# Performance work log

Hardware: AMD Instinct MI355X
Metric: run time of the kernel (lower is better)

## Reference

```python
import jax, jax.numpy as jnp
import numpy as np
from jax import lax

BN_EPS = 1e-5


def conv_bn_relu(x, W, g, b, m, v):
    # 3x3 conv, pad=1, stride=1, no bias; then inference-mode BN; then ReLU
    y = lax.conv_general_dilated(x, W, (1, 1), 'SAME',
                                 dimension_numbers=('NCHW', 'OIHW', 'NCHW'))
    scale = g / jnp.sqrt(v + BN_EPS)
    y = y * scale[None, :, None, None] + (b - m * scale)[None, :, None, None]
    return jax.nn.relu(y)


def shifted_windows(y, d, pad_val):
    # y: [n,c,h,w] -> [k*k, n, c, h, w] of all spatial shifts within radius d
    n, c, h, w = y.shape
    yp = jnp.pad(y, ((0, 0), (0, 0), (d, d), (d, d)), constant_values=pad_val)
    k = 2 * d + 1
    return jnp.stack([yp[:, :, i:i + h, j:j + w] for i in range(k) for j in range(k)], axis=0)


def setup_inputs() -> dict:
    key = jax.random.key(0)
    ks = jax.random.split(key, 16)
    n_clip, n, C_in, H, W = 2, 2, 512, 64, 64
    emb_dim, fc_dim, num_class = 256, 128, 124

    def bn_params(k, c):
        k1, k2, k3, k4 = jax.random.split(k, 4)
        return (jax.random.uniform(k1, (c,)) + 0.5,
                jax.random.normal(k2, (c,)) * 0.1,
                jax.random.normal(k3, (c,)) * 0.1,
                jax.random.uniform(k4, (c,)) + 0.5)

    emb_g, emb_b, emb_m, emb_v = bn_params(ks[0], emb_dim)
    emb2_g, emb2_b, emb2_m, emb2_v = bn_params(ks[1], fc_dim)
    return {
        'clip_embs': jax.random.normal(ks[2], (n_clip * n, C_in, H, W), dtype=jnp.float32),
        'clip_num': 2,
        'emb_W': jax.random.normal(ks[3], (emb_dim, C_in, 3, 3), dtype=jnp.float32) * 0.02,
        'emb_g': emb_g, 'emb_b': emb_b, 'emb_m': emb_m, 'emb_v': emb_v,
        'emb2_W': jax.random.normal(ks[4], (fc_dim, C_in, 3, 3), dtype=jnp.float32) * 0.02,
        'emb2_g': emb2_g, 'emb2_b': emb2_b, 'emb2_m': emb2_m, 'emb2_v': emb2_v,
        'last_W': jax.random.normal(ks[5], (num_class, emb_dim, 1, 1), dtype=jnp.float32) * 0.05,
        'last_b': jnp.zeros((num_class,), dtype=jnp.float32),
    }


MAX_DISTANCES = (2,)
TEMP = 1.0


def reference(clip_embs, clip_num, emb_W, emb_g, emb_b, emb_m, emb_v,
              emb2_W, emb2_g, emb2_b, emb2_m, emb2_v, last_W, last_b):
    # emb_2 features used for the local cost volume (fc_dim channels)
    clip_emb2 = conv_bn_relu(clip_embs, emb2_W, emb2_g, emb2_b, emb2_m, emb2_v)
    chunks2 = jnp.split(clip_emb2, clip_num, axis=0)
    c2 = chunks2[-1]                      # current frame, [n, fc_dim, h, w]
    others2 = chunks2[:-1]

    x2 = jnp.sum(c2 * c2, axis=1)         # [n,h,w]

    all_weights = []                       # per other clip: per max_distance softmax weights
    for other in others2:
        y2 = jnp.sum(other * other, axis=1, keepdims=True)  # [n,1,h,w]
        w_list = []
        for d in MAX_DISTANCES:
            k = 2 * d + 1
            y_sh = shifted_windows(other, d, 0.0)            # [k2,n,c,h,w]
            y2_sh = shifted_windows(y2, d, 1e20)[:, :, 0]    # [k2,n,h,w]
            cross = jnp.einsum('nchw,onchw->onhw', c2, y_sh)
            dist = x2[None] + y2_sh - 2.0 * cross            # [k2,n,h,w] squared L2
            # distsoftmax branch: softmax over the k*k window of 1/(dist*temp+1e-5)
            w_ = jax.nn.softmax(1.0 / (dist * TEMP + 1e-5), axis=0)
            w_list.append(w_)
        all_weights.append(w_list)

    # emb features (emb_dim channels) that get warped
    clip_emb_s = conv_bn_relu(clip_embs, emb_W, emb_g, emb_b, emb_m, emb_v)
    chunks_s = jnp.split(clip_emb_s, clip_num, axis=0)
    c_img = chunks_s[-1]                   # [n, emb_dim, h, w]
    others_s = chunks_s[:-1]

    final_emb = [c_img]
    for other, w_list in zip(others_s, all_weights):
        warp_fs = []
        for d, w_ in zip(MAX_DISTANCES, w_list):
            k = 2 * d + 1
            o_sh = shifted_windows(other, d, 0.0)            # [k2,n,c,h,w]
            # weighted sum over window, then avgpool over k*k -> divide by k*k
            warp = jnp.einsum('onchw,onhw->nchw', o_sh, w_) / (k * k)
            warp_fs.append(warp)
        final_emb.append(jnp.mean(jnp.stack(warp_fs, axis=-1), axis=-1))

    # linear_combine=False: mean over the clip embeddings
    final_fea = jnp.mean(jnp.stack(final_emb, axis=-1), axis=-1)

    # last_layer: dropout (eval -> identity) + 1x1 conv
    logits = jnp.einsum('nchw,oc->nohw', final_fea, last_W[:, :, 0, 0]) + last_b[None, :, None, None]
    x = jax.nn.log_softmax(logits, axis=1)
    return (x, clip_emb2)
```

## Files before the change

### kernel.cpp

```cpp
#include <hip/hip_runtime.h>
#include <hip/hip_bf16.h>
#include <stdint.h>


typedef float v4f __attribute__((ext_vector_type(4)));
typedef __bf16 v8bf __attribute__((ext_vector_type(8)));
typedef unsigned short u16;
typedef unsigned int u32;
typedef u16 u16x8 __attribute__((ext_vector_type(8)));

constexpr size_t XH_OFF  = 0;
constexpr size_t XH_BYTES = (size_t)4*66*66*512*2;
constexpr size_t WT_OFF  = XH_OFF + XH_BYTES;
constexpr size_t WT_BYTES = (size_t)9*16*24*64*8*2;
constexpr size_t FS_OFF  = WT_OFF + WT_BYTES;
constexpr size_t FS_BYTES = (size_t)4*68*68*256*2;
constexpr size_t F2_OFF  = FS_OFF + FS_BYTES;
constexpr size_t F2_BYTES = (size_t)4*68*68*128*4;
constexpr size_t Y2_OFF  = F2_OFF + F2_BYTES;
constexpr size_t Y2_BYTES = (size_t)2*68*68*4;
constexpr size_t FEA_OFF = Y2_OFF + Y2_BYTES;
constexpr size_t FEA_BYTES = (size_t)2*4096*256*2;
constexpr size_t WL_OFF  = FEA_OFF + FEA_BYTES;
constexpr size_t WL_BYTES = (size_t)128*256*2;
constexpr size_t SC_OFF  = WL_OFF + WL_BYTES;
constexpr size_t WS_TOTAL = SC_OFF + 768*4;

__device__ __forceinline__ float bf2f(u16 h) { return __uint_as_float(((u32)h) << 16); }
__device__ __forceinline__ u16 f2bf(float f) {
  u32 u = __float_as_uint(f);
  return (u16)((u + 0x7fffu + ((u >> 16) & 1u)) >> 16);
}

__device__ __forceinline__ void gld16(const void* g, const void* l) {
  __builtin_amdgcn_global_load_lds(
      (const __attribute__((address_space(1))) void*)(uintptr_t)g,
      (__attribute__((address_space(3))) void*)(u32)(uintptr_t)l,
      16, 0, 0);
}

__global__ void k_init(const float* __restrict__ eg, const float* __restrict__ eb,
                       const float* __restrict__ em, const float* __restrict__ ev,
                       const float* __restrict__ e2g, const float* __restrict__ e2b,
                       const float* __restrict__ e2m, const float* __restrict__ e2v,
                       const float* __restrict__ lw,
                       u16* __restrict__ Xh, u16* __restrict__ Fs, float* __restrict__ F2,
                       float* __restrict__ Y2, u16* __restrict__ Wl,
                       float* __restrict__ sc, float* __restrict__ bi) {
  const u32 N0 = 4u * 260u * 64u;
  const u32 N1 = 4u * 528u * 32u;
  const u32 N2 = 4u * 528u * 32u;
  const u32 N3 = 2u * 68u * 68u;
  const u32 N4 = 4096u;
  const u32 N5 = 384u;
  const u32 TOT = N0 + N1 + N2 + N3 + N4 + N5;
  const u16x8 z8 = {0,0,0,0,0,0,0,0};
  for (u32 i = blockIdx.x * 256u + threadIdx.x; i < TOT; i += gridDim.x * 256u) {
    if (i < N0) {
      const u32 img = i / (260u * 64u);
      const u32 rem = i - img * (260u * 64u);
      const u32 r = rem >> 6, ch8 = rem & 63u;
      u32 prow, pcol;
      if (r < 132u) { prow = (r >= 66u) ? 65u : 0u; pcol = r - ((r >= 66u) ? 66u : 0u); }
      else { const u32 rr = r - 132u; prow = 1u + (rr >> 1); pcol = (rr & 1u) * 65u; }
      *(u16x8*)(Xh + ((size_t)((img * 66u + prow) * 66u + pcol)) * 512u + ch8 * 8u) = z8;
    } else if (i < N0 + N1 + N2) {
      const bool isF2 = (i >= N0 + N1);
      const u32 j = isF2 ? (i - N0 - N1) : (i - N0);
      const u32 img = j / (528u * 32u);
      const u32 rem = j - img * (528u * 32u);
      const u32 r = rem >> 5, cg = rem & 31u;
      u32 prow, pcol;
      if (r < 272u) { const u32 q = r / 68u; prow = (q < 2u) ? q : q + 64u; pcol = r - q * 68u; }
      else { const u32 rr = r - 272u; prow = 2u + (rr >> 2); const u32 c = rr & 3u; pcol = (c < 2u) ? c : c + 64u; }
      if (isF2) {
        const float4 zf = {0.f, 0.f, 0.f, 0.f};
        *(float4*)(F2 + ((size_t)((img * 68u + prow) * 68u + pcol)) * 128u + cg * 4u) = zf;
      } else {
        *(u16x8*)(Fs + ((size_t)((img * 68u + prow) * 68u + pcol)) * 256u + cg * 8u) = z8;
      }
    } else if (i < N0 + N1 + N2 + N3) {
      const u32 j = i - N0 - N1 - N2;
      const u32 n = j / 4624u, rc = j - n * 4624u;
      const u32 rr = rc / 68u, cc = rc - rr * 68u;
      const bool interior = (rr >= 2u && rr < 66u && cc >= 2u && cc < 66u);
      Y2[j] = interior ? 0.f : 1e20f;
    } else if (i < N0 + N1 + N2 + N3 + N4) {
      const u32 j = i - N0 - N1 - N2 - N3;
      const u32 row = j >> 5, c8 = (j & 31u) * 8u;
      u16x8 o;
      #pragma unroll
      for (int k = 0; k < 8; ++k) o[k] = (row < 124u) ? f2bf(lw[row * 256u + c8 + k]) : (u16)0;
      *(u16x8*)(Wl + (size_t)row * 256u + c8) = o;
    } else {
      const u32 id = i - N0 - N1 - N2 - N3 - N4;
      float g, b, m, v;
      if (id < 256u) { g = eg[id]; b = eb[id]; m = em[id]; v = ev[id]; }
      else { const u32 q = id - 256u; g = e2g[q]; b = e2b[q]; m = e2m[q]; v = e2v[q]; }
      const float s = g / sqrtf(v + 1e-5f);
      sc[id] = s;
      bi[id] = b - m * s;
    }
  }
}

__global__ __launch_bounds__(256) void k_prep_x(const float* __restrict__ X, u16* __restrict__ Xh) {
  __shared__ __align__(16) float tile[64 * 65];
  const int tid = threadIdx.x;
  const int n = blockIdx.x >> 7;
  const int rem = blockIdx.x & 127;
  const int h = rem >> 1, chalf = rem & 1;
  const int wq = tid >> 6, wcol = tid & 63;
  #pragma unroll 1
  for (int it = 0; it < 4; ++it) {
    const int c0 = chalf * 256 + it * 64;
    __syncthreads();
    #pragma unroll
    for (int i = 0; i < 16; ++i) {
      const int cl = i * 4 + wq;
      tile[cl * 65 + wcol] = X[((size_t)(n * 512 + c0 + cl)) * 4096 + h * 64 + wcol];
    }
    __syncthreads();
    const int w = tid >> 2, cg = tid & 3;
    u16x8 a, b;
    #pragma unroll
    for (int j = 0; j < 8; ++j) a[j] = f2bf(tile[(cg * 16 + j) * 65 + w]);
    #pragma unroll
    for (int j = 0; j < 8; ++j) b[j] = f2bf(tile[(cg * 16 + 8 + j) * 65 + w]);
    u16* dst = Xh + ((size_t)((n * 66 + h + 1) * 66 + (w + 1))) * 512 + c0 + cg * 16;
    *(u16x8*)dst = a;
    *((u16x8*)dst + 1) = b;
  }
}

__global__ __launch_bounds__(256) void k_prep_w(const float* __restrict__ embW, const float* __restrict__ emb2W,
                                                u16* __restrict__ Wf) {
  __shared__ float row[4608];
  const int oc = blockIdx.x;
  const int tid = threadIdx.x;
  const float* src = (oc < 256) ? (embW + (size_t)oc * 4608) : (emb2W + (size_t)(oc - 256) * 4608);
  for (int i = tid; i < 4608; i += 256) row[i] = src[i];
  __syncthreads();
  const int cc = tid >> 4;
  const int slot = (tid >> 2) & 3;
  const int e = 2 * (tid & 3);
  const int r = oc & 15, ocb = oc >> 4;
  #pragma unroll
  for (int pos = 0; pos < 9; ++pos) {
    const u32 pk = (u32)f2bf(row[(2 * tid) * 9 + pos]) | ((u32)f2bf(row[(2 * tid + 1) * 9 + pos]) << 16);
    *(u32*)(Wf + ((size_t)((pos * 16 + cc) * 24 + ocb)) * 512 + (slot * 16 + r) * 8 + e) = pk;
  }
}

__global__ __launch_bounds__(256) void k_conv(const u16* __restrict__ Xh, const u16* __restrict__ Wf,
                                              const float* __restrict__ sc, const float* __restrict__ bi,
                                              float* __restrict__ out2, float* __restrict__ F2,
                                              u16* __restrict__ Fs, float* __restrict__ Y2) {
  __shared__ __align__(16) char lds[34816];
  const int tid = threadIdx.x;
  const int wvi = tid >> 6, lane = tid & 63;
  const int octile = blockIdx.x >> 7;
  const int rest = blockIdx.x & 127;
  const int n = rest >> 5, pt = rest & 31;
  const int h0 = pt * 2;
  const int ochalf = wvi >> 1, prow = wvi & 1;

  float* scl = (float*)(lds + 33792);
  float* bil = scl + 128;
  if (tid < 128) { scl[tid] = sc[octile * 128 + tid]; bil[tid] = bi[octile * 128 + tid]; }

  const u16* xbase = Xh + (size_t)n * 66 * 66 * 512;
  int bofs[5];
  #pragma unroll
  for (int k = 0; k < 5; ++k) {
    const int idx = k * 256 + tid;
    if (idx < 1056) {
      const int col = idx >> 2;
      const int ssrc = (idx & 3) ^ ((col >> 1) & 3);
      const int imgrow = col / 66, c = col - imgrow * 66;
      bofs[k] = ((h0 + imgrow) * 66 + c) * 512 + ssrc * 8;
    } else bofs[k] = 0;
  }

  auto stageB = [&](int cc, int buf) {
    char* base = lds + buf * 16896;
    #pragma unroll
    for (int k = 0; k < 4; ++k)
      gld16(xbase + bofs[k] + cc * 32, base + k * 4096 + tid * 16);
    if (tid < 32) gld16(xbase + bofs[4] + cc * 32, base + 16384 + tid * 16);
  };

  const int ocb0 = octile * 8 + ochalf * 4;
  const int lane8 = lane * 8;
  auto loadA = [&](int pos, int cc, int mt) {
    return *(const v8bf*)(Wf + ((size_t)((pos * 16 + cc) * 24 + ocb0 + mt)) * 512 + lane8);
  };
  const int rbB = prow * 66 + (lane & 15);
  const int slotb = lane >> 4;
  auto readB = [&](int buf, int rb) {
    return *(const v8bf*)(lds + buf * 16896 + rb * 64 + (((slotb ^ ((rb >> 1) & 3))) << 4));
  };

  v4f acc[4][4];
  #pragma unroll
  for (int mt = 0; mt < 4; ++mt)
    #pragma unroll
    for (int nt = 0; nt < 4; ++nt) acc[mt][nt] = (v4f){0.f, 0.f, 0.f, 0.f};

  int buf = 0;
  stageB(0, 0);
  v8bf ac[4];
  #pragma unroll
  for (int mt = 0; mt < 4; ++mt) ac[mt] = loadA(0, 0, mt);
  __syncthreads();

  #pragma unroll 1
  for (int cc = 0; cc < 16; ++cc) {
    #pragma unroll
    for (int pos = 0; pos < 9; ++pos) {
      const int ky = pos / 3, kx = pos % 3;
      if (pos == 5 && cc < 15) stageB(cc + 1, buf ^ 1);
      v8bf an[4];
      if (pos < 8) {
        #pragma unroll
        for (int mt = 0; mt < 4; ++mt) an[mt] = loadA(pos + 1, cc, mt);
      } else if (cc < 15) {
        #pragma unroll
        for (int mt = 0; mt < 4; ++mt) an[mt] = loadA(0, cc + 1, mt);
      } else {
        #pragma unroll
        for (int mt = 0; mt < 4; ++mt) an[mt] = ac[mt];
      }
      v8bf bfr[4];
      #pragma unroll
      for (int nt = 0; nt < 4; ++nt)
        bfr[nt] = readB(buf, rbB + ky * 66 + kx + nt * 16);
      #pragma unroll
      for (int mt = 0; mt < 4; ++mt)
        #pragma unroll
        for (int nt = 0; nt < 4; ++nt)
          acc[mt][nt] = __builtin_amdgcn_mfma_f32_16x16x32_bf16(ac[mt], bfr[nt], acc[mt][nt], 0, 0, 0);
      if (pos == 8) { __syncthreads(); buf ^= 1; }
      #pragma unroll
      for (int mt = 0; mt < 4; ++mt) ac[mt] = an[mt];
    }
  }

  float vals[4][4][4];
  #pragma unroll
  for (int mt = 0; mt < 4; ++mt) {
    const int ocb = ochalf * 64 + mt * 16 + ((lane >> 4) << 2);
    #pragma unroll
    for (int j = 0; j < 4; ++j) {
      const float s = scl[ocb + j], tt = bil[ocb + j];
      #pragma unroll
      for (int nt = 0; nt < 4; ++nt) vals[mt][nt][j] = fmaxf(fmaf(acc[mt][nt][j], s, tt), 0.f);
    }
  }

  if (octile == 2) {
    #pragma unroll
    for (int mt = 0; mt < 4; ++mt)
      #pragma unroll
      for (int j = 0; j < 4; ++j) {
        const int ocl = ochalf * 64 + mt * 16 + ((lane >> 4) << 2) + j;
        float* orow = out2 + ((size_t)(n * 128 + ocl)) * 4096 + (h0 + prow) * 64;
        #pragma unroll
        for (int nt = 0; nt < 4; ++nt) orow[nt * 16 + (lane & 15)] = vals[mt][nt][j];
      }
    if (n < 2) {
      #pragma unroll
      for (int nt = 0; nt < 4; ++nt) {
        float s = 0.f;
        #pragma unroll
        for (int mt = 0; mt < 4; ++mt)
          #pragma unroll
          for (int j = 0; j < 4; ++j) s = fmaf(vals[mt][nt][j], vals[mt][nt][j], s);
        s += __shfl_xor(s, 16);
        s += __shfl_xor(s, 32);
        if ((lane >> 4) == 0)
          atomicAdd(&Y2[(size_t)(n * 68 + h0 + prow + 2) * 68 + nt * 16 + (lane & 15) + 2], s);
      }
    }
    float* T = (float*)lds;
    #pragma unroll 1
    for (int mr = 0; mr < 2; ++mr) {
      __syncthreads();
      if (ochalf == mr) {
        #pragma unroll
        for (int mt = 0; mt < 4; ++mt)
          #pragma unroll
          for (int nt = 0; nt < 4; ++nt) {
            const int p = prow * 64 + nt * 16 + (lane & 15);
            #pragma unroll
            for (int j = 0; j < 4; ++j) {
              const int c = mt * 16 + ((lane >> 4) << 2) + j;
              T[p * 64 + (((c >> 2) ^ (p & 15)) << 2) + (c & 3)] = vals[mt][nt][j];
            }
          }
      }
      __syncthreads();
      const int p = tid >> 1, half = tid & 1;
      float* dst = F2 + ((size_t)((n * 68 + h0 + (p >> 6) + 2) * 68 + (p & 63) + 2)) * 128 + mr * 64 + half * 32;
      #pragma unroll
      for (int i = 0; i < 8; ++i) {
        const int s = (half * 8 + i) ^ (p & 15);
        *(float4*)(dst + i * 4) = *(const float4*)(T + p * 64 + s * 4);
      }
    }
  } else {
    u16* T = (u16*)lds;
    #pragma unroll
    for (int mt = 0; mt < 4; ++mt)
      #pragma unroll
      for (int nt = 0; nt < 4; ++nt) {
        const int p = prow * 64 + nt * 16 + (lane & 15);
        #pragma unroll
        for (int jj = 0; jj < 2; ++jj) {
          const u32 pk = (u32)f2bf(vals[mt][nt][2 * jj]) | ((u32)f2bf(vals[mt][nt][2 * jj + 1]) << 16);
          const int c = ochalf * 64 + mt * 16 + ((lane >> 4) << 2) + 2 * jj;
          *(u32*)(T + p * 128 + (((c >> 3) ^ (p & 15)) << 3) + (c & 7)) = pk;
        }
      }
    __syncthreads();
    const int p = tid >> 1, half = tid & 1;
    u16* dst = Fs + ((size_t)((n * 68 + h0 + (p >> 6) + 2) * 68 + (p & 63) + 2)) * 256 + octile * 128 + half * 64;
    #pragma unroll
    for (int i = 0; i < 8; ++i) {
      const int s = (half * 8 + i) ^ (p & 15);
      *(u16x8*)(dst + i * 8) = *(const u16x8*)(T + p * 128 + s * 8);
    }
  }
}

__global__ __launch_bounds__(256) void k_dw(const float* __restrict__ F2, const float* __restrict__ Y2,
                                            const u16* __restrict__ Fs, u16* __restrict__ Fea) {
  const int t = blockIdx.x * 256 + threadIdx.x;
  const int g = t & 15;
  const int px = t >> 4;
  const int n = px >> 12;
  const int p = px & 4095;
  const int h = p >> 6, w = p & 63;

  const float4* c2p = (const float4*)(F2 + ((size_t)(((n + 2) * 68 + h + 2) * 68 + (w + 2))) * 128 + g * 8);
  float4 c2v[2];
  float x2 = 0.f;
  #pragma unroll
  for (int i = 0; i < 2; ++i) {
    c2v[i] = c2p[i];
    x2 += c2v[i].x * c2v[i].x + c2v[i].y * c2v[i].y + c2v[i].z * c2v[i].z + c2v[i].w * c2v[i].w;
  }
  float cross[25];
  #pragma unroll
  for (int dy = 0; dy < 5; ++dy) {
    const float* rowp = F2 + ((size_t)((n * 68 + h + dy) * 68 + w)) * 128 + g * 8;
    #pragma unroll
    for (int dx = 0; dx < 5; ++dx) {
      const float4* wp = (const float4*)(rowp + dx * 128);
      float s = 0.f;
      #pragma unroll
      for (int i = 0; i < 2; ++i) {
        const float4 u = wp[i];
        s += c2v[i].x * u.x + c2v[i].y * u.y + c2v[i].z * u.z + c2v[i].w * u.w;
      }
      cross[dy * 5 + dx] = s;
    }
  }
  x2 += __shfl_xor(x2, 1); x2 += __shfl_xor(x2, 2); x2 += __shfl_xor(x2, 4); x2 += __shfl_xor(x2, 8);
  #pragma unroll
  for (int o = 0; o < 25; ++o) {
    cross[o] += __shfl_xor(cross[o], 1);
    cross[o] += __shfl_xor(cross[o], 2);
    cross[o] += __shfl_xor(cross[o], 4);
    cross[o] += __shfl_xor(cross[o], 8);
  }
  float wv[25], mx = -1e30f;
  #pragma unroll
  for (int dy = 0; dy < 5; ++dy)
    #pragma unroll
    for (int dx = 0; dx < 5; ++dx) {
      const int o = dy * 5 + dx;
      const float y2v = Y2[(size_t)(n * 68 + h + dy) * 68 + (w + dx)];
      const float dist = x2 + y2v - 2.f * cross[o];
// ... 80 lines not shown
  for (int mt = 0; mt < 8; ++mt)
    #pragma unroll
    for (int j = 0; j < 4; ++j) {
      const int cls = mt * 16 + r0 + j;
      if (cls < 124) s += __expf(v[mt][j] - mx);
    }
  s += __shfl_xor(s, 16);
  s += __shfl_xor(s, 32);
  const float lz = mx + logf(s);
  #pragma unroll
  for (int mt = 0; mt < 8; ++mt)
    #pragma unroll
    for (int j = 0; j < 4; ++j) {
      const int cls = mt * 16 + r0 + j;
      if (cls < 124)
        xout[((size_t)(n * 124 + cls)) * 4096 + p0 + lp] = v[mt][j] - lz;
    }
}

extern "C" void kernel_launch(void* const* d_in, const int* in_sizes, int n_in,
                              void* d_out, int out_size, void* d_ws, size_t ws_size,
                              hipStream_t stream) {
  (void)in_sizes; (void)n_in; (void)out_size;
  const float* clip  = (const float*)d_in[0];
  const float* embW  = (const float*)d_in[2];
  const float* eg    = (const float*)d_in[3];
  const float* eb    = (const float*)d_in[4];
  const float* em    = (const float*)d_in[5];
  const float* ev    = (const float*)d_in[6];
  const float* emb2W = (const float*)d_in[7];
  const float* e2g   = (const float*)d_in[8];
  const float* e2b   = (const float*)d_in[9];
  const float* e2m   = (const float*)d_in[10];
  const float* e2v   = (const float*)d_in[11];
  const float* lw    = (const float*)d_in[12];
  const float* lb    = (const float*)d_in[13];

  char* ws = (char*)d_ws;
  u16*   Xh  = (u16*)(ws + XH_OFF);
  u16*   Wf  = (u16*)(ws + WT_OFF);
  u16*   Fs  = (u16*)(ws + FS_OFF);
  float* F2  = (float*)(ws + F2_OFF);
  float* Y2  = (float*)(ws + Y2_OFF);
  u16*   Fea = (u16*)(ws + FEA_OFF);
  u16*   Wl  = (u16*)(ws + WL_OFF);
  float* sc  = (float*)(ws + SC_OFF);
  float* bi  = sc + 384;

  float* xout = (float*)d_out;
  float* out2 = xout + (size_t)2 * 124 * 64 * 64;

  if (ws_size < WS_TOTAL) return;

  k_init<<<256, 256, 0, stream>>>(eg, eb, em, ev, e2g, e2b, e2m, e2v, lw, Xh, Fs, F2, Y2, Wl, sc, bi);
  k_prep_x<<<512, 256, 0, stream>>>(clip, Xh);
  k_prep_w<<<384, 256, 0, stream>>>(embW, emb2W, Wf);
  k_conv<<<384, 256, 0, stream>>>(Xh, Wf, sc, bi, out2, F2, Fs, Y2);
  k_dw<<<512, 256, 0, stream>>>(F2, Y2, Fs, Fea);
  k_logits<<<256, 128, 0, stream>>>(Fea, Wl, lb, xout);
}
```

Before: 221.5 us.

## Retile conv to 192-channel by one-row blocks with LDS-staged weights

The implicit-GEMM conv kernel now runs 512 blocks of two waves, each block covering one output row and 192 output channels (96 per wave). It used to run 384 blocks of four waves covering two rows and 128 channels. Weight fragments are now double-buffered through LDS with async global-to-LDS loads instead of being read into registers directly from global memory. The epilogue is rebuilt so the second channel tile writes both the tail of the bf16 emb features and the fp32 emb2 outputs. Each B tile is reused across more output channels, but the kernel now takes a barrier on every kernel position, uses more LDS, and holds more accumulators per wave.

```diff
diff --git a/kernel.cpp b/kernel.cpp
--- a/kernel.cpp
+++ b/kernel.cpp
@@ -152,104 +152,102 @@
   }
 }
 
-__global__ __launch_bounds__(256) void k_conv(const u16* __restrict__ Xh, const u16* __restrict__ Wf,
+__global__ __launch_bounds__(128) void k_conv(const u16* __restrict__ Xh, const u16* __restrict__ Wf,
                                               const float* __restrict__ sc, const float* __restrict__ bi,
                                               float* __restrict__ out2, float* __restrict__ F2,
                                               u16* __restrict__ Fs, float* __restrict__ Y2) {
-  __shared__ __align__(16) char lds[34816];
+  __shared__ __align__(16) char lds[51456];
   const int tid = threadIdx.x;
-  const int wvi = tid >> 6, lane = tid & 63;
-  const int octile = blockIdx.x >> 7;
-  const int rest = blockIdx.x & 127;
-  const int n = rest >> 5, pt = rest & 31;
-  const int h0 = pt * 2;
-  const int ochalf = wvi >> 1, prow = wvi & 1;
-
-  float* scl = (float*)(lds + 33792);
-  float* bil = scl + 128;
-  if (tid < 128) { scl[tid] = sc[octile * 128 + tid]; bil[tid] = bi[octile * 128 + tid]; }
+  const int wv = tid >> 6, lane = tid & 63;
+  const int octile = blockIdx.x >> 8;
+  const int rest = blockIdx.x & 255;
+  const int n = rest >> 6, h = rest & 63;
+  const int oc0b = octile * 12;
+
+  float* scl = (float*)(lds + 49920);
+  float* bil = scl + 192;
+  for (int i = tid; i < 192; i += 128) {
+    scl[i] = sc[octile * 192 + i];
+    bil[i] = bi[octile * 192 + i];
+  }
 
   const u16* xbase = Xh + (size_t)n * 66 * 66 * 512;
-  int bofs[5];
-  #pragma unroll
-  for (int k = 0; k < 5; ++k) {
-    const int idx = k * 256 + tid;
-    if (idx < 1056) {
+  int bofs[7];
+  #pragma unroll
+  for (int k = 0; k < 7; ++k) {
+    const int idx = k * 128 + tid;
+    if (idx < 792) {
       const int col = idx >> 2;
       const int ssrc = (idx & 3) ^ ((col >> 1) & 3);
       const int imgrow = col / 66, c = col - imgrow * 66;
-      bofs[k] = ((h0 + imgrow) * 66 + c) * 512 + ssrc * 8;
+      bofs[k] = ((h + imgrow) * 66 + c) * 512 + ssrc * 8;
     } else bofs[k] = 0;
   }
 
+  auto stageA = [&](int pos, int cc, int buf) {
+    const u16* base = Wf + ((size_t)((pos * 16 + cc) * 24 + oc0b)) * 512;
+    #pragma unroll
+    for (int k = 0; k < 6; ++k) {
+      const int frag = 2 * k + wv;
+      gld16(base + frag * 512 + lane * 8, lds + buf * 12288 + (frag * 64 + lane) * 16);
+    }
+  };
   auto stageB = [&](int cc, int buf) {
-    char* base = lds + buf * 16896;
-    #pragma unroll
-    for (int k = 0; k < 4; ++k)
-      gld16(xbase + bofs[k] + cc * 32, base + k * 4096 + tid * 16);
-    if (tid < 32) gld16(xbase + bofs[4] + cc * 32, base + 16384 + tid * 16);
+    char* base = lds + 24576 + buf * 12672;
+    #pragma unroll
+    for (int k = 0; k < 6; ++k)
+      gld16(xbase + bofs[k] + cc * 32, base + (k * 128 + tid) * 16);
+    if (tid < 24) gld16(xbase + bofs[6] + cc * 32, base + (768 + tid) * 16);
   };
 
-  const int ocb0 = octile * 8 + ochalf * 4;
-  const int lane8 = lane * 8;
-  auto loadA = [&](int pos, int cc, int mt) {
-    return *(const v8bf*)(Wf + ((size_t)((pos * 16 + cc) * 24 + ocb0 + mt)) * 512 + lane8);
-  };
-  const int rbB = prow * 66 + (lane & 15);
+  v4f acc[6][4];
+  #pragma unroll
+  for (int mt = 0; mt < 6; ++mt)
+    #pragma unroll
+    for (int nt = 0; nt < 4; ++nt) acc[mt][nt] = (v4f){0.f, 0.f, 0.f, 0.f};
+
+  int bA = 0, bB = 0;
+  stageB(0, 0);
+  stageA(0, 0, 0);
+  __syncthreads();
+
+  const int r0 = lane & 15;
   const int slotb = lane >> 4;
-  auto readB = [&](int buf, int rb) {
-    return *(const v8bf*)(lds + buf * 16896 + rb * 64 + (((slotb ^ ((rb >> 1) & 3))) << 4));
-  };
-
-  v4f acc[4][4];
-  #pragma unroll
-  for (int mt = 0; mt < 4; ++mt)
-    #pragma unroll
-    for (int nt = 0; nt < 4; ++nt) acc[mt][nt] = (v4f){0.f, 0.f, 0.f, 0.f};
-
-  int buf = 0;
-  stageB(0, 0);
-  v8bf ac[4];
-  #pragma unroll
-  for (int mt = 0; mt < 4; ++mt) ac[mt] = loadA(0, 0, mt);
-  __syncthreads();
+  const char* ldsB = lds + 24576;
 
   #pragma unroll 1
   for (int cc = 0; cc < 16; ++cc) {
     #pragma unroll
     for (int pos = 0; pos < 9; ++pos) {
       const int ky = pos / 3, kx = pos % 3;
-      if (pos == 5 && cc < 15) stageB(cc + 1, buf ^ 1);
-      v8bf an[4];
-      if (pos < 8) {
-        #pragma unroll
-        for (int mt = 0; mt < 4; ++mt) an[mt] = loadA(pos + 1, cc, mt);
-      } else if (cc < 15) {
-        #pragma unroll
-        for (int mt = 0; mt < 4; ++mt) an[mt] = loadA(0, cc + 1, mt);
-      } else {
-        #pragma unroll
-        for (int mt = 0; mt < 4; ++mt) an[mt] = ac[mt];
+      if (pos == 5 && cc < 15) stageB(cc + 1, bB ^ 1);
+      if (pos < 8) stageA(pos + 1, cc, bA ^ 1);
+      else if (cc < 15) stageA(0, cc + 1, bA ^ 1);
+      v8bf af[6], bf4[4];
+      const char* pA = lds + bA * 12288 + wv * 6144 + lane * 16;
+      #pragma unroll
+      for (int mt = 0; mt < 6; ++mt) af[mt] = *(const v8bf*)(pA + mt * 1024);
+      #pragma unroll
+      for (int nt = 0; nt < 4; ++nt) {
+        const int rb = ky * 66 + kx + nt * 16 + r0;
+        bf4[nt] = *(const v8bf*)(ldsB + bB * 12672 + rb * 64 + ((slotb ^ ((rb >> 1) & 3)) << 4));
       }
-      v8bf bfr[4];
-      #pragma unroll
-      for (int nt = 0; nt < 4; ++nt)
-        bfr[nt] = readB(buf, rbB + ky * 66 + kx + nt * 16);
-      #pragma unroll
-      for (int mt = 0; mt < 4; ++mt)
+      #pragma unroll
+      for (int mt = 0; mt < 6; ++mt)
         #pragma unroll
         for (int nt = 0; nt < 4; ++nt)
-          acc[mt][nt] = __builtin_amdgcn_mfma_f32_16x16x32_bf16(ac[mt], bfr[nt], acc[mt][nt], 0, 0, 0);
-      if (pos == 8) { __syncthreads(); buf ^= 1; }
-      #pragma unroll
-      for (int mt = 0; mt < 4; ++mt) ac[mt] = an[mt];
-    }
-  }
-
-  float vals[4][4][4];
-  #pragma unroll
-  for (int mt = 0; mt < 4; ++mt) {
-    const int ocb = ochalf * 64 + mt * 16 + ((lane >> 4) << 2);
+          acc[mt][nt] = __builtin_amdgcn_mfma_f32_16x16x32_bf16(af[mt], bf4[nt], acc[mt][nt], 0, 0, 0);
+      __syncthreads();
+      bA ^= 1;
+      if (pos == 8) bB ^= 1;
+    }
+  }
+
+  const int q4 = (lane >> 4) << 2;
+  float vals[6][4][4];
+  #pragma unroll
+  for (int mt = 0; mt < 6; ++mt) {
+    const int ocb = wv * 96 + mt * 16 + q4;
     #pragma unroll
     for (int j = 0; j < 4; ++j) {
       const float s = scl[ocb + j], tt = bil[ocb + j];
@@ -258,77 +256,88 @@
     }
   }
 
-  if (octile == 2) {
-    #pragma unroll
-    for (int mt = 0; mt < 4; ++mt)
-      #pragma unroll
-      for (int j = 0; j < 4; ++j) {
-        const int ocl = ochalf * 64 + mt * 16 + ((lane >> 4) << 2) + j;
-        float* orow = out2 + ((size_t)(n * 128 + ocl)) * 4096 + (h0 + prow) * 64;
-        #pragma unroll
-        for (int nt = 0; nt < 4; ++nt) orow[nt * 16 + (lane & 15)] = vals[mt][nt][j];
-      }
-    if (n < 2) {
+  if (octile == 0) {
+    u16* T = (u16*)lds;
+    #pragma unroll
+    for (int mt = 0; mt < 6; ++mt)
       #pragma unroll
       for (int nt = 0; nt < 4; ++nt) {
-        float s = 0.f;
-        #pragma unroll
-        for (int mt = 0; mt < 4; ++mt)
-          #pragma unroll
-          for (int j = 0; j < 4; ++j) s = fmaf(vals[mt][nt][j], vals[mt][nt][j], s);
-        s += __shfl_xor(s, 16);
-        s += __shfl_xor(s, 32);
-        if ((lane >> 4) == 0)
-          atomicAdd(&Y2[(size_t)(n * 68 + h0 + prow + 2) * 68 + nt * 16 + (lane & 15) + 2], s);
-      }
-    }
-    float* T = (float*)lds;
-    #pragma unroll 1
-    for (int mr = 0; mr < 2; ++mr) {
-      __syncthreads();
-      if (ochalf == mr) {
-        #pragma unroll
-        for (int mt = 0; mt < 4; ++mt)
-          #pragma unroll
-          for (int nt = 0; nt < 4; ++nt) {
-            const int p = prow * 64 + nt * 16 + (lane & 15);
-            #pragma unroll
-            for (int j = 0; j < 4; ++j) {
-              const int c = mt * 16 + ((lane >> 4) << 2) + j;
-              T[p * 64 + (((c >> 2) ^ (p & 15)) << 2) + (c & 3)] = vals[mt][nt][j];
-            }
-          }
-      }
-      __syncthreads();
-      const int p = tid >> 1, half = tid & 1;
-      float* dst = F2 + ((size_t)((n * 68 + h0 + (p >> 6) + 2) * 68 + (p & 63) + 2)) * 128 + mr * 64 + half * 32;
-      #pragma unroll
-      for (int i = 0; i < 8; ++i) {
-        const int s = (half * 8 + i) ^ (p & 15);
-        *(float4*)(dst + i * 4) = *(const float4*)(T + p * 64 + s * 4);
-      }
-    }
-  } else {
-    u16* T = (u16*)lds;
-    #pragma unroll
-    for (int mt = 0; mt < 4; ++mt)
-      #pragma unroll
-      for (int nt = 0; nt < 4; ++nt) {
-        const int p = prow * 64 + nt * 16 + (lane & 15);
+        const int p = nt * 16 + r0;
         #pragma unroll
         for (int jj = 0; jj < 2; ++jj) {
           const u32 pk = (u32)f2bf(vals[mt][nt][2 * jj]) | ((u32)f2bf(vals[mt][nt][2 * jj + 1]) << 16);
-          const int c = ochalf * 64 + mt * 16 + ((lane >> 4) << 2) + 2 * jj;
-          *(u32*)(T + p * 128 + (((c >> 3) ^ (p & 15)) << 3) + (c & 7)) = pk;
+          const int c = wv * 96 + mt * 16 + q4 + 2 * jj;
+          *(u32*)(T + p * 256 + (((c >> 3) ^ (p & 15)) << 3) + (c & 7)) = pk;
         }
       }
     __syncthreads();
     const int p = tid >> 1, half = tid & 1;
-    u16* dst = Fs + ((size_t)((n * 68 + h0 + (p >> 6) + 2) * 68 + (p & 63) + 2)) * 256 + octile * 128 + half * 64;
-    #pragma unroll
-    for (int i = 0; i < 8; ++i) {
-      const int s = (half * 8 + i) ^ (p & 15);
-      *(u16x8*)(dst + i * 8) = *(const u16x8*)(T + p * 128 + s * 8);
+    u16* dst = Fs + ((size_t)((n * 68 + h + 2) * 68 + p + 2)) * 256 + half * 96;
+    #pragma unroll
+    for (int i = 0; i < 12; ++i) {
+      const int cs = half * 12 + i;
+      *(u16x8*)(dst + i * 8) = *(const u16x8*)(T + p * 256 + ((cs ^ (p & 15)) << 3));
+    }
+  } else {
+    float* T = (float*)lds;
+    u16* T2 = (u16*)(lds + 32768);
+    #pragma unroll
+    for (int mt = 0; mt < 6; ++mt) {
+      const int fb = 192 + wv * 96 + mt * 16;
+      if (fb >= 256) {
+        #pragma unroll
+        for (int j = 0; j < 4; ++j) {
+          float* orow = out2 + ((size_t)(n * 128 + fb - 256 + q4 + j)) * 4096 + h * 64;
+          #pragma unroll
+          for (int nt = 0; nt < 4; ++nt) orow[nt * 16 + r0] = vals[mt][nt][j];
+        }
+        if (n < 2) {
+          #pragma unroll
+          for (int nt = 0; nt < 4; ++nt) {
+            float s = 0.f;
+            #pragma unroll
+            for (int j = 0; j < 4; ++j) s = fmaf(vals[mt][nt][j], vals[mt][nt][j], s);
+            s += __shfl_xor(s, 16);
+            s += __shfl_xor(s, 32);
+            if ((lane >> 4) == 0)
+              atomicAdd(&Y2[(size_t)(n * 68 + h + 2) * 68 + nt * 16 + r0 + 2], s);
+          }
+        }
+        #pragma unroll
+        for (int nt = 0; nt < 4; ++nt) {
+          const int p = nt * 16 + r0;
+          #pragma unroll
+          for (int j = 0; j < 4; ++j) {
+            const int c = fb - 256 + q4 + j;
+            T[p * 128 + (((c >> 2) ^ (p & 15)) << 2) + (c & 3)] = vals[mt][nt][j];
+          }
+        }
+      } else {
+        #pragma unroll
+        for (int nt = 0; nt < 4; ++nt) {
+          const int p = nt * 16 + r0;
+          #pragma unroll
+          for (int jj = 0; jj < 2; ++jj) {
+            const u32 pk = (u32)f2bf(vals[mt][nt][2 * jj]) | ((u32)f2bf(vals[mt][nt][2 * jj + 1]) << 16);
+            const int c = mt * 16 + q4 + 2 * jj;
+            *(u32*)(T2 + p * 64 + (((c >> 3) ^ (p & 7)) << 3) + (c & 7)) = pk;
+          }
+        }
+      }
+    }
+    __syncthreads();
+    const int p = tid >> 1, half = tid & 1;
+    float* f2dst = F2 + ((size_t)((n * 68 + h + 2) * 68 + p + 2)) * 128 + half * 64;
+    #pragma unroll
+    for (int i = 0; i < 16; ++i) {
+      const int cs = half * 16 + i;
+      *(float4*)(f2dst + i * 4) = *(const float4*)(T + p * 128 + ((cs ^ (p & 15)) << 2));
+    }
+    u16* fsdst = Fs + ((size_t)((n * 68 + h + 2) * 68 + p + 2)) * 256 + 192 + half * 32;
+    #pragma unroll
+    for (int i = 0; i < 4; ++i) {
+      const int cs = half * 4 + i;
+      *(u16x8*)(fsdst + i * 8) = *(const u16x8*)(T2 + p * 64 + ((cs ^ (p & 7)) << 3));
     }
   }
 }
@@ -518,7 +527,7 @@
   k_init<<<256, 256, 0, stream>>>(eg, eb, em, ev, e2g, e2b, e2m, e2v, lw, Xh, Fs, F2, Y2, Wl, sc, bi);
   k_prep_x<<<512, 256, 0, stream>>>(clip, Xh);
   k_prep_w<<<384, 256, 0, stream>>>(embW, emb2W, Wf);
-  k_conv<<<384, 256, 0, stream>>>(Xh, Wf, sc, bi, out2, F2, Fs, Y2);
+  k_conv<<<512, 128, 0, stream>>>(Xh, Wf, sc, bi, out2, F2, Fs, Y2);
   k_dw<<<512, 256, 0, stream>>>(F2, Y2, Fs, Fea);
   k_logits<<<256, 128, 0, stream>>>(Fea, Wl, lb, xout);
 }
```

After: 217.6 us. About the same (-1.8%).

## Merge prep kernels and retile conv to 64-channel tiles with LDS-staged weights

Applied to the files above, without the earlier changes.

The three preparation kernels (padding init, input transpose to bf16, weight repack) are merged into one launch dispatched by block index, which removes two kernel launches. The conv kernel now tiles 64 output channels per block instead of 128, doubling the grid to 768 blocks for better CU occupancy. Weight fragments are staged into LDS through double-buffered global_load_lds instead of direct global register loads. The cost is a block-wide barrier after every kernel position instead of once per channel chunk, and each input tile is loaded twice as many times across blocks.

```diff
diff --git a/kernel.cpp b/kernel.cpp
--- a/kernel.cpp
+++ b/kernel.cpp
@@ -39,116 +39,118 @@
       16, 0, 0);
 }
 
-__global__ void k_init(const float* __restrict__ eg, const float* __restrict__ eb,
+__global__ __launch_bounds__(256) void k_prep(const float* __restrict__ X,
+                       const float* __restrict__ embW, const float* __restrict__ emb2W,
+                       const float* __restrict__ eg, const float* __restrict__ eb,
                        const float* __restrict__ em, const float* __restrict__ ev,
                        const float* __restrict__ e2g, const float* __restrict__ e2b,
                        const float* __restrict__ e2m, const float* __restrict__ e2v,
                        const float* __restrict__ lw,
-                       u16* __restrict__ Xh, u16* __restrict__ Fs, float* __restrict__ F2,
+                       u16* __restrict__ Xh, u16* __restrict__ Wf,
+                       u16* __restrict__ Fs, float* __restrict__ F2,
                        float* __restrict__ Y2, u16* __restrict__ Wl,
                        float* __restrict__ sc, float* __restrict__ bi) {
-  const u32 N0 = 4u * 260u * 64u;
-  const u32 N1 = 4u * 528u * 32u;
-  const u32 N2 = 4u * 528u * 32u;
-  const u32 N3 = 2u * 68u * 68u;
-  const u32 N4 = 4096u;
-  const u32 N5 = 384u;
-  const u32 TOT = N0 + N1 + N2 + N3 + N4 + N5;
-  const u16x8 z8 = {0,0,0,0,0,0,0,0};
-  for (u32 i = blockIdx.x * 256u + threadIdx.x; i < TOT; i += gridDim.x * 256u) {
-    if (i < N0) {
-      const u32 img = i / (260u * 64u);
-      const u32 rem = i - img * (260u * 64u);
-      const u32 r = rem >> 6, ch8 = rem & 63u;
-      u32 prow, pcol;
-      if (r < 132u) { prow = (r >= 66u) ? 65u : 0u; pcol = r - ((r >= 66u) ? 66u : 0u); }
-      else { const u32 rr = r - 132u; prow = 1u + (rr >> 1); pcol = (rr & 1u) * 65u; }
-      *(u16x8*)(Xh + ((size_t)((img * 66u + prow) * 66u + pcol)) * 512u + ch8 * 8u) = z8;
-    } else if (i < N0 + N1 + N2) {
-      const bool isF2 = (i >= N0 + N1);
-      const u32 j = isF2 ? (i - N0 - N1) : (i - N0);
-      const u32 img = j / (528u * 32u);
-      const u32 rem = j - img * (528u * 32u);
-      const u32 r = rem >> 5, cg = rem & 31u;
-      u32 prow, pcol;
-      if (r < 272u) { const u32 q = r / 68u; prow = (q < 2u) ? q : q + 64u; pcol = r - q * 68u; }
-      else { const u32 rr = r - 272u; prow = 2u + (rr >> 2); const u32 c = rr & 3u; pcol = (c < 2u) ? c : c + 64u; }
-      if (isF2) {
-        const float4 zf = {0.f, 0.f, 0.f, 0.f};
-        *(float4*)(F2 + ((size_t)((img * 68u + prow) * 68u + pcol)) * 128u + cg * 4u) = zf;
+  __shared__ __align__(16) char shbuf[18688];
+  const int bid = blockIdx.x;
+  const int tid = threadIdx.x;
+  if (bid < 256) {
+    const u32 N0 = 4u * 260u * 64u;
+    const u32 N1 = 4u * 528u * 32u;
+    const u32 N2 = 4u * 528u * 32u;
+    const u32 N3 = 2u * 68u * 68u;
+    const u32 N4 = 4096u;
+    const u32 N5 = 384u;
+    const u32 TOT = N0 + N1 + N2 + N3 + N4 + N5;
+    const u16x8 z8 = {0,0,0,0,0,0,0,0};
+    for (u32 i = bid * 256u + tid; i < TOT; i += 65536u) {
+      if (i < N0) {
+        const u32 img = i / (260u * 64u);
+        const u32 rem = i - img * (260u * 64u);
+        const u32 r = rem >> 6, ch8 = rem & 63u;
+        u32 prow, pcol;
+        if (r < 132u) { prow = (r >= 66u) ? 65u : 0u; pcol = r - ((r >= 66u) ? 66u : 0u); }
+        else { const u32 rr = r - 132u; prow = 1u + (rr >> 1); pcol = (rr & 1u) * 65u; }
+        *(u16x8*)(Xh + ((size_t)((img * 66u + prow) * 66u + pcol)) * 512u + ch8 * 8u) = z8;
+      } else if (i < N0 + N1 + N2) {
+        const bool isF2 = (i >= N0 + N1);
+        const u32 j = isF2 ? (i - N0 - N1) : (i - N0);
+        const u32 img = j / (528u * 32u);
+        const u32 rem = j - img * (528u * 32u);
+        const u32 r = rem >> 5, cg = rem & 31u;
+        u32 prow, pcol;
+        if (r < 272u) { const u32 q = r / 68u; prow = (q < 2u) ? q : q + 64u; pcol = r - q * 68u; }
+        else { const u32 rr = r - 272u; prow = 2u + (rr >> 2); const u32 c = rr & 3u; pcol = (c < 2u) ? c : c + 64u; }
+        if (isF2) {
+          const float4 zf = {0.f, 0.f, 0.f, 0.f};
+          *(float4*)(F2 + ((size_t)((img * 68u + prow) * 68u + pcol)) * 128u + cg * 4u) = zf;
+        } else {
+          *(u16x8*)(Fs + ((size_t)((img * 68u + prow) * 68u + pcol)) * 256u + cg * 8u) = z8;
+        }
+      } else if (i < N0 + N1 + N2 + N3) {
+        const u32 j = i - N0 - N1 - N2;
+        const u32 n = j / 4624u, rc = j - n * 4624u;
+        const u32 rr = rc / 68u, cc = rc - rr * 68u;
+        const bool interior = (rr >= 2u && rr < 66u && cc >= 2u && cc < 66u);
+        Y2[j] = interior ? 0.f : 1e20f;
+      } else if (i < N0 + N1 + N2 + N3 + N4) {
+        const u32 j = i - N0 - N1 - N2 - N3;
+        const u32 row = j >> 5, c8 = (j & 31u) * 8u;
+        u16x8 o;
+        #pragma unroll
+        for (int k = 0; k < 8; ++k) o[k] = (row < 124u) ? f2bf(lw[row * 256u + c8 + k]) : (u16)0;
+        *(u16x8*)(Wl + (size_t)row * 256u + c8) = o;
       } else {
-        *(u16x8*)(Fs + ((size_t)((img * 68u + prow) * 68u + pcol)) * 256u + cg * 8u) = z8;
-      }
-    } else if (i < N0 + N1 + N2 + N3) {
-      const u32 j = i - N0 - N1 - N2;
-      const u32 n = j / 4624u, rc = j - n * 4624u;
-      const u32 rr = rc / 68u, cc = rc - rr * 68u;
-      const bool interior = (rr >= 2u && rr < 66u && cc >= 2u && cc < 66u);
-      Y2[j] = interior ? 0.f : 1e20f;
-    } else if (i < N0 + N1 + N2 + N3 + N4) {
-      const u32 j = i - N0 - N1 - N2 - N3;
-      const u32 row = j >> 5, c8 = (j & 31u) * 8u;
-      u16x8 o;
-      #pragma unroll
-      for (int k = 0; k < 8; ++k) o[k] = (row < 124u) ? f2bf(lw[row * 256u + c8 + k]) : (u16)0;
-      *(u16x8*)(Wl + (size_t)row * 256u + c8) = o;
-    } else {
-      const u32 id = i - N0 - N1 - N2 - N3 - N4;
-      float g, b, m, v;
-      if (id < 256u) { g = eg[id]; b = eb[id]; m = em[id]; v = ev[id]; }
-      else { const u32 q = id - 256u; g = e2g[q]; b = e2b[q]; m = e2m[q]; v = e2v[q]; }
-      const float s = g / sqrtf(v + 1e-5f);
-      sc[id] = s;
-      bi[id] = b - m * s;
-    }
-  }
-}
-
-__global__ __launch_bounds__(256) void k_prep_x(const float* __restrict__ X, u16* __restrict__ Xh) {
-  __shared__ __align__(16) float tile[64 * 65];
-  const int tid = threadIdx.x;
-  const int n = blockIdx.x >> 7;
-  const int rem = blockIdx.x & 127;
-  const int h = rem >> 1, chalf = rem & 1;
-  const int wq = tid >> 6, wcol = tid & 63;
-  #pragma unroll 1
-  for (int it = 0; it < 4; ++it) {
-    const int c0 = chalf * 256 + it * 64;
+        const u32 id = i - N0 - N1 - N2 - N3 - N4;
+        float g, b, m, v;
+        if (id < 256u) { g = eg[id]; b = eb[id]; m = em[id]; v = ev[id]; }
+        else { const u32 q = id - 256u; g = e2g[q]; b = e2b[q]; m = e2m[q]; v = e2v[q]; }
+        const float s = g / sqrtf(v + 1e-5f);
+        sc[id] = s;
+        bi[id] = b - m * s;
+      }
+    }
+  } else if (bid < 768) {
+    float* tile = (float*)shbuf;
+    const int b2 = bid - 256;
+    const int n = b2 >> 7;
+    const int rem = b2 & 127;
+    const int h = rem >> 1, chalf = rem & 1;
+    const int wq = tid >> 6, wcol = tid & 63;
+    #pragma unroll 1
+    for (int it = 0; it < 4; ++it) {
+      const int c0 = chalf * 256 + it * 64;
+      __syncthreads();
+      #pragma unroll
+      for (int i = 0; i < 16; ++i) {
+        const int cl = i * 4 + wq;
+        tile[cl * 65 + wcol] = X[((size_t)(n * 512 + c0 + cl)) * 4096 + h * 64 + wcol];
+      }
+      __syncthreads();
+      const int w = tid >> 2, cg = tid & 3;
+      u16x8 a, b;
+      #pragma unroll
+      for (int j = 0; j < 8; ++j) a[j] = f2bf(tile[(cg * 16 + j) * 65 + w]);
+      #pragma unroll
+      for (int j = 0; j < 8; ++j) b[j] = f2bf(tile[(cg * 16 + 8 + j) * 65 + w]);
+      u16* dst = Xh + ((size_t)((n * 66 + h + 1) * 66 + (w + 1))) * 512 + c0 + cg * 16;
+      *(u16x8*)dst = a;
+      *((u16x8*)dst + 1) = b;
+    }
+  } else {
+    float* row = (float*)shbuf;
+    const int oc = bid - 768;
+    const float* src = (oc < 256) ? (embW + (size_t)oc * 4608) : (emb2W + (size_t)(oc - 256) * 4608);
+    for (int i = tid; i < 4608; i += 256) row[i] = src[i];
     __syncthreads();
-    #pragma unroll
-    for (int i = 0; i < 16; ++i) {
-      const int cl = i * 4 + wq;
-      tile[cl * 65 + wcol] = X[((size_t)(n * 512 + c0 + cl)) * 4096 + h * 64 + wcol];
-    }
-    __syncthreads();
-    const int w = tid >> 2, cg = tid & 3;
-    u16x8 a, b;
-    #pragma unroll
-    for (int j = 0; j < 8; ++j) a[j] = f2bf(tile[(cg * 16 + j) * 65 + w]);
-    #pragma unroll
-    for (int j = 0; j < 8; ++j) b[j] = f2bf(tile[(cg * 16 + 8 + j) * 65 + w]);
-    u16* dst = Xh + ((size_t)((n * 66 + h + 1) * 66 + (w + 1))) * 512 + c0 + cg * 16;
-    *(u16x8*)dst = a;
-    *((u16x8*)dst + 1) = b;
-  }
-}
-
-__global__ __launch_bounds__(256) void k_prep_w(const float* __restrict__ embW, const float* __restrict__ emb2W,
-                                                u16* __restrict__ Wf) {
-  __shared__ float row[4608];
-  const int oc = blockIdx.x;
-  const int tid = threadIdx.x;
-  const float* src = (oc < 256) ? (embW + (size_t)oc * 4608) : (emb2W + (size_t)(oc - 256) * 4608);
-  for (int i = tid; i < 4608; i += 256) row[i] = src[i];
-  __syncthreads();
-  const int cc = tid >> 4;
-  const int slot = (tid >> 2) & 3;
-  const int e = 2 * (tid & 3);
-  const int r = oc & 15, ocb = oc >> 4;
-  #pragma unroll
-  for (int pos = 0; pos < 9; ++pos) {
-    const u32 pk = (u32)f2bf(row[(2 * tid) * 9 + pos]) | ((u32)f2bf(row[(2 * tid + 1) * 9 + pos]) << 16);
-    *(u32*)(Wf + ((size_t)((pos * 16 + cc) * 24 + ocb)) * 512 + (slot * 16 + r) * 8 + e) = pk;
+    const int cc = tid >> 4;
+    const int slot = (tid >> 2) & 3;
+    const int e = 2 * (tid & 3);
+    const int r = oc & 15, ocb = oc >> 4;
+    #pragma unroll
+    for (int pos = 0; pos < 9; ++pos) {
+      const u32 pk = (u32)f2bf(row[(2 * tid) * 9 + pos]) | ((u32)f2bf(row[(2 * tid + 1) * 9 + pos]) << 16);
+      *(u32*)(Wf + ((size_t)((pos * 16 + cc) * 24 + ocb)) * 512 + (slot * 16 + r) * 8 + e) = pk;
+    }
   }
 }
 
@@ -156,18 +158,20 @@
                                               const float* __restrict__ sc, const float* __restrict__ bi,
                                               float* __restrict__ out2, float* __restrict__ F2,
                                               u16* __restrict__ Fs, float* __restrict__ Y2) {
-  __shared__ __align__(16) char lds[34816];
+  __shared__ __align__(16) char lds[42496];
   const int tid = threadIdx.x;
-  const int wvi = tid >> 6, lane = tid & 63;
+  const int wv = tid >> 6, lane = tid & 63;
   const int octile = blockIdx.x >> 7;
   const int rest = blockIdx.x & 127;
   const int n = rest >> 5, pt = rest & 31;
   const int h0 = pt * 2;
-  const int ochalf = wvi >> 1, prow = wvi & 1;
-
-  float* scl = (float*)(lds + 33792);
-  float* bil = scl + 128;
-  if (tid < 128) { scl[tid] = sc[octile * 128 + tid]; bil[tid] = bi[octile * 128 + tid]; }
+  const int ocb0 = octile * 4;
+  const int pxrow = wv >> 1;
+  const int pxc0 = (wv & 1) * 32;
+
+  float* scl = (float*)(lds + 41984);
+  float* bil = scl + 64;
+  if (tid < 64) { scl[tid] = sc[octile * 64 + tid]; bil[tid] = bi[octile * 64 + tid]; }
 
   const u16* xbase = Xh + (size_t)n * 66 * 66 * 512;
   int bofs[5];
@@ -182,95 +186,109 @@
     } else bofs[k] = 0;
   }
 
+  auto stageA = [&](int pos, int cc, int buf) {
+    gld16(Wf + ((size_t)((pos * 16 + cc) * 24 + ocb0)) * 512 + tid * 8, lds + buf * 4096 + tid * 16);
+  };
   auto stageB = [&](int cc, int buf) {
-    char* base = lds + buf * 16896;
+    char* base = lds + 8192 + buf * 16896;
     #pragma unroll
     for (int k = 0; k < 4; ++k)
       gld16(xbase + bofs[k] + cc * 32, base + k * 4096 + tid * 16);
     if (tid < 32) gld16(xbase + bofs[4] + cc * 32, base + 16384 + tid * 16);
   };
 
-  const int ocb0 = octile * 8 + ochalf * 4;
-  const int lane8 = lane * 8;
-  auto loadA = [&](int pos, int cc, int mt) {
-    return *(const v8bf*)(Wf + ((size_t)((pos * 16 + cc) * 24 + ocb0 + mt)) * 512 + lane8);
-  };
-  const int rbB = prow * 66 + (lane & 15);
+  v4f acc[4][2];
+  #pragma unroll
+  for (int mt = 0; mt < 4; ++mt) { acc[mt][0] = (v4f){0,0,0,0}; acc[mt][1] = (v4f){0,0,0,0}; }
+
+  int bA = 0, bB = 0;
+  stageB(0, 0);
+  stageA(0, 0, 0);
+  __syncthreads();
+
+  const int r0 = lane & 15;
   const int slotb = lane >> 4;
-  auto readB = [&](int buf, int rb) {
-    return *(const v8bf*)(lds + buf * 16896 + rb * 64 + (((slotb ^ ((rb >> 1) & 3))) << 4));
-  };
-
-  v4f acc[4][4];
-  #pragma unroll
-  for (int mt = 0; mt < 4; ++mt)
-    #pragma unroll
-    for (int nt = 0; nt < 4; ++nt) acc[mt][nt] = (v4f){0.f, 0.f, 0.f, 0.f};
-
-  int buf = 0;
-  stageB(0, 0);
-  v8bf ac[4];
-  #pragma unroll
-  for (int mt = 0; mt < 4; ++mt) ac[mt] = loadA(0, 0, mt);
-  __syncthreads();
+  const char* ldsB = lds + 8192;
 
   #pragma unroll 1
   for (int cc = 0; cc < 16; ++cc) {
     #pragma unroll
     for (int pos = 0; pos < 9; ++pos) {
       const int ky = pos / 3, kx = pos % 3;
-      if (pos == 5 && cc < 15) stageB(cc + 1, buf ^ 1);
-      v8bf an[4];
       if (pos < 8) {
-        #pragma unroll
-        for (int mt = 0; mt < 4; ++mt) an[mt] = loadA(pos + 1, cc, mt);
+        stageA(pos + 1, cc, bA ^ 1);
       } else if (cc < 15) {
-        #pragma unroll
-        for (int mt = 0; mt < 4; ++mt) an[mt] = loadA(0, cc + 1, mt);
-      } else {
-        #pragma unroll
-        for (int mt = 0; mt < 4; ++mt) an[mt] = ac[mt];
-      }
-      v8bf bfr[4];
-      #pragma unroll
-      for (int nt = 0; nt < 4; ++nt)
-        bfr[nt] = readB(buf, rbB + ky * 66 + kx + nt * 16);
+        stageB(cc + 1, bB ^ 1);
+        stageA(0, cc + 1, bA ^ 1);
+      }
+      v8bf af[4], bfr[2];
+      const char* pA = lds + bA * 4096 + lane * 16;
+      #pragma unroll
+      for (int mt = 0; mt < 4; ++mt) af[mt] = *(const v8bf*)(pA + mt * 1024);
+      #pragma unroll
+      for (int nt = 0; nt < 2; ++nt) {
+        const int rb = (pxrow + ky) * 66 + pxc0 + nt * 16 + r0 + kx;
+        bfr[nt] = *(const v8bf*)(ldsB + bB * 16896 + rb * 64 + ((slotb ^ ((rb >> 1) & 3)) << 4));
+      }
       #pragma unroll
       for (int mt = 0; mt < 4; ++mt)
         #pragma unroll
-        for (int nt = 0; nt < 4; ++nt)
-          acc[mt][nt] = __builtin_amdgcn_mfma_f32_16x16x32_bf16(ac[mt], bfr[nt], acc[mt][nt], 0, 0, 0);
-      if (pos == 8) { __syncthreads(); buf ^= 1; }
-      #pragma unroll
-      for (int mt = 0; mt < 4; ++mt) ac[mt] = an[mt];
-    }
-  }
-
-  float vals[4][4][4];
+        for (int nt = 0; nt < 2; ++nt)
+          acc[mt][nt] = __builtin_amdgcn_mfma_f32_16x16x32_bf16(af[mt], bfr[nt], acc[mt][nt], 0, 0, 0);
+      __syncthreads();
+      bA ^= 1;
+      if (pos == 8) bB ^= 1;
+    }
+  }
+
+  const int q4 = (lane >> 4) << 2;
+  float vals[4][2][4];
   #pragma unroll
   for (int mt = 0; mt < 4; ++mt) {
-    const int ocb = ochalf * 64 + mt * 16 + ((lane >> 4) << 2);
+    const int ocb = mt * 16 + q4;
     #pragma unroll
     for (int j = 0; j < 4; ++j) {
       const float s = scl[ocb + j], tt = bil[ocb + j];
       #pragma unroll
-      for (int nt = 0; nt < 4; ++nt) vals[mt][nt][j] = fmaxf(fmaf(acc[mt][nt][j], s, tt), 0.f);
-    }
-  }
-
-  if (octile == 2) {
+      for (int nt = 0; nt < 2; ++nt) vals[mt][nt][j] = fmaxf(fmaf(acc[mt][nt][j], s, tt), 0.f);
+    }
+  }
+
+  if (octile < 4) {
+    u16* T = (u16*)lds;
     #pragma unroll
     for (int mt = 0; mt < 4; ++mt)
       #pragma unroll
+      for (int nt = 0; nt < 2; ++nt) {
+        const int p = pxrow * 64 + pxc0 + nt * 16 + r0;
+        #pragma unroll
+        for (int jj = 0; jj < 2; ++jj) {
+          const int c = mt * 16 + q4 + 2 * jj;
+          *(u32*)(T + p * 64 + (((c >> 3) ^ (p & 7)) << 3) + (c & 7)) =
+              (u32)f2bf(vals[mt][nt][2 * jj]) | ((u32)f2bf(vals[mt][nt][2 * jj + 1]) << 16);
+        }
+      }
+    __syncthreads();
+    const int p = tid >> 1, half = tid & 1;
+    u16* dst = Fs + ((size_t)((n * 68 + h0 + (p >> 6) + 2) * 68 + (p & 63) + 2)) * 256 + octile * 64 + half * 32;
+    #pragma unroll
+    for (int i = 0; i < 4; ++i) {
+      const int cs = half * 4 + i;
+      *(u16x8*)(dst + i * 8) = *(const u16x8*)(T + p * 64 + ((cs ^ (p & 7)) << 3));
+    }
+  } else {
+    #pragma unroll
+    for (int mt = 0; mt < 4; ++mt)
+      #pragma unroll
       for (int j = 0; j < 4; ++j) {
-        const int ocl = ochalf * 64 + mt * 16 + ((lane >> 4) << 2) + j;
-        float* orow = out2 + ((size_t)(n * 128 + ocl)) * 4096 + (h0 + prow) * 64;
-        #pragma unroll
-        for (int nt = 0; nt < 4; ++nt) orow[nt * 16 + (lane & 15)] = vals[mt][nt][j];
+        const int ocl = (octile - 4) * 64 + mt * 16 + q4 + j;
+        float* orow = out2 + ((size_t)(n * 128 + ocl)) * 4096 + (h0 + pxrow) * 64 + pxc0;
+        orow[r0] = vals[mt][0][j];
+        orow[16 + r0] = vals[mt][1][j];
       }
     if (n < 2) {
       #pragma unroll
-      for (int nt = 0; nt < 4; ++nt) {
+      for (int nt = 0; nt < 2; ++nt) {
         float s = 0.f;
         #pragma unroll
         for (int mt = 0; mt < 4; ++mt)
@@ -279,56 +297,28 @@
         s += __shfl_xor(s, 16);
         s += __shfl_xor(s, 32);
         if ((lane >> 4) == 0)
-          atomicAdd(&Y2[(size_t)(n * 68 + h0 + prow + 2) * 68 + nt * 16 + (lane & 15) + 2], s);
+          atomicAdd(&Y2[(size_t)(n * 68 + h0 + pxrow + 2) * 68 + pxc0 + nt * 16 + r0 + 2], s);
       }
     }
     float* T = (float*)lds;
-    #pragma unroll 1
-    for (int mr = 0; mr < 2; ++mr) {
-      __syncthreads();
-      if (ochalf == mr) {
+    #pragma unroll
+    for (int mt = 0; mt < 4; ++mt)
+      #pragma unroll
+      for (int nt = 0; nt < 2; ++nt) {
+        const int p = pxrow * 64 + pxc0 + nt * 16 + r0;
         #pragma unroll
-        for (int mt = 0; mt < 4; ++mt)
-          #pragma unroll
-          for (int nt = 0; nt < 4; ++nt) {
-            const int p = prow * 64 + nt * 16 + (lane & 15);
-            #pragma unroll
-            for (int j = 0; j < 4; ++j) {
-              const int c = mt * 16 + ((lane >> 4) << 2) + j;
-              T[p * 64 + (((c >> 2) ^ (p & 15)) << 2) + (c & 3)] = vals[mt][nt][j];
-            }
-          }
-      }
-      __syncthreads();
-      const int p = tid >> 1, half = tid & 1;
-      float* dst = F2 + ((size_t)((n * 68 + h0 + (p >> 6) + 2) * 68 + (p & 63) + 2)) * 128 + mr * 64 + half * 32;
-      #pragma unroll
-      for (int i = 0; i < 8; ++i) {
-        const int s = (half * 8 + i) ^ (p & 15);
-        *(float4*)(dst + i * 4) = *(const float4*)(T + p * 64 + s * 4);
-      }
-    }
-  } else {
-    u16* T = (u16*)lds;
-    #pragma unroll
-    for (int mt = 0; mt < 4; ++mt)
-      #pragma unroll
-      for (int nt = 0; nt < 4; ++nt) {
-        const int p = prow * 64 + nt * 16 + (lane & 15);
-        #pragma unroll
-        for (int jj = 0; jj < 2; ++jj) {
-          const u32 pk = (u32)f2bf(vals[mt][nt][2 * jj]) | ((u32)f2bf(vals[mt][nt][2 * jj + 1]) << 16);
-          const int c = ochalf * 64 + mt * 16 + ((lane >> 4) << 2) + 2 * jj;
-          *(u32*)(T + p * 128 + (((c >> 3) ^ (p & 15)) << 3) + (c & 7)) = pk;
+        for (int j = 0; j < 4; ++j) {
+          const int c = mt * 16 + q4 + j;
+          T[p * 64 + (((c >> 2) ^ (p & 15)) << 2) + (c & 3)] = vals[mt][nt][j];
         }
       }
     __syncthreads();
     const int p = tid >> 1, half = tid & 1;
-    u16* dst = Fs + ((size_t)((n * 68 + h0 + (p >> 6) + 2) * 68 + (p & 63) + 2)) * 256 + octile * 128 + half * 64;
+    float* dst = F2 + ((size_t)((n * 68 + h0 + (p >> 6) + 2) * 68 + (p & 63) + 2)) * 128 + (octile - 4) * 64 + half * 32;
     #pragma unroll
     for (int i = 0; i < 8; ++i) {
-      const int s = (half * 8 + i) ^ (p & 15);
-      *(u16x8*)(dst + i * 8) = *(const u16x8*)(T + p * 128 + s * 8);
+      const int cs = half * 8 + i;
+      *(float4*)(dst + i * 4) = *(const float4*)(T + p * 64 + ((cs ^ (p & 15)) << 2));
     }
   }
 }
@@ -515,10 +505,9 @@
 
   if (ws_size < WS_TOTAL) return;
 
-  k_init<<<256, 256, 0, stream>>>(eg, eb, em, ev, e2g, e2b, e2m, e2v, lw, Xh, Fs, F2, Y2, Wl, sc, bi);
-  k_prep_x<<<512, 256, 0, stream>>>(clip, Xh);
-  k_prep_w<<<384, 256, 0, stream>>>(embW, emb2W, Wf);
-  k_conv<<<384, 256, 0, stream>>>(Xh, Wf, sc, bi, out2, F2, Fs, Y2);
+  k_prep<<<1152, 256, 0, stream>>>(clip, embW, emb2W, eg, eb, em, ev, e2g, e2b, e2m, e2v, lw,
+                                   Xh, Wf, Fs, F2, Y2, Wl, sc, bi);
+  k_conv<<<768, 256, 0, stream>>>(Xh, Wf, sc, bi, out2, F2, Fs, Y2);
   k_dw<<<512, 256, 0, stream>>>(F2, Y2, Fs, Fea);
   k_logits<<<256, 128, 0, stream>>>(Fea, Wl, lb, xout);
 }
```

Result: faster. 192.5 us (-13.1%).
